# Kernel optimization log

Measured on AMD Instinct MI355X. Metric: run time of the kernel, lower is better.

Reference implementation:

```python
import jax, jax.numpy as jnp
import numpy as np

# JAX reference for BERN-NN-Implicit LayerModule.forward.
# Semantics: for each output node i,
#   combined_over[i]  = sum_j relu(W)[i,j]*inputs_over[j] + (-relu(-W))[i,j]*inputs_under[j] + bias[i]
#   combined_under[i] = sum_j (-relu(-W))[i,j]*inputs_over[j] + relu(W)[i,j]*inputs_under[j] + bias[i]
# With all input Bernstein polynomials at equal degree, SumModule reduces to addition
# and prod_input_weights reduces to a weighted sum over the previous-layer neuron axis.

N_IN = 64      # previous-layer neurons
SIZE = 64      # nodes in this layer
G = 513        # Bernstein coefficient grid per dim (degree 512 + 1), dims = 2


def setup_inputs() -> dict:
    key = jax.random.key(0)
    k1, k2, k3, k4 = jax.random.split(key, 4)
    return {
        "inputs_under": jax.random.normal(k1, (N_IN, G, G), dtype=jnp.float32),
        "inputs_over": jax.random.normal(k2, (N_IN, G, G), dtype=jnp.float32),
        "weights": jax.random.normal(k3, (SIZE, N_IN), dtype=jnp.float32),
        "biases": jax.random.normal(k4, (SIZE,), dtype=jnp.float32),
        "layer_idx": 0,
    }


def reference(inputs_under, inputs_over, weights, biases, layer_idx):
    w_pos = jax.nn.relu(weights)          # [size, n_in]
    w_neg = -jax.nn.relu(-weights)        # [size, n_in]
    b = biases[:, None, None]             # [size, 1, 1]
    # [size, G, G] Bernstein coefficient grids per output node
    combined_over = (jnp.einsum("oi,ixy->oxy", w_pos, inputs_over)
                     + jnp.einsum("oi,ixy->oxy", w_neg, inputs_under)) + b
    combined_under = (jnp.einsum("oi,ixy->oxy", w_neg, inputs_over)
                      + jnp.einsum("oi,ixy->oxy", w_pos, inputs_under)) + b
    return combined_under, combined_over
```

## Files before the change

kernel.cpp:

```cpp
#include <hip/hip_runtime.h>

constexpr int PIX   = 513 * 513;
constexpr int NTILE = 128;

typedef short bf16x8 __attribute__((ext_vector_type(8)));
typedef float f32x4  __attribute__((ext_vector_type(4)));

__device__ unsigned short g_Wbig[128 * 128];

__device__ __forceinline__ unsigned short f2bf(float f) {
    unsigned u = __builtin_bit_cast(unsigned, f);
    u += 0x7fffu + ((u >> 16) & 1u);
    return (unsigned short)(u >> 16);
}
__device__ __forceinline__ unsigned pack2(float a, float b) {
    return (unsigned)f2bf(a) | ((unsigned)f2bf(b) << 16);
}

__global__ __launch_bounds__(256) void prep_kernel(const float* __restrict__ W) {
    const int idx = blockIdx.x * 256 + threadIdx.x;
    const int m = idx >> 7, k = idx & 127;
    const float w = W[(m & 63) * 64 + (k & 63)];
    const bool same = ((m < 64) == (k < 64));
    g_Wbig[idx] = f2bf(same ? fmaxf(w, 0.f) : fminf(w, 0.f));
}

__global__ __launch_bounds__(512, 4) void mfma_bounds_kernel(
    const float* __restrict__ under,
    const float* __restrict__ over,
    const float* __restrict__ W,
    const float* __restrict__ bias,
    float* __restrict__ out_under,
    float* __restrict__ out_over)
{
    __shared__ alignas(16) unsigned short Xt[NTILE * 128];

    const int t = threadIdx.x;
    const int pxbase = blockIdx.x * NTILE;

    if (pxbase + NTILE > PIX) {
        if (t < 128) {
            const int m = t;
            const int o = m & 63;
            const float* prim = (m < 64) ? over  : under;
            const float* sec  = (m < 64) ? under : over;
            for (int p = pxbase; p < PIX; ++p) {
                float acc = bias[o];
                for (int i = 0; i < 64; ++i) {
                    const float w = W[o * 64 + i];
                    acc += fmaxf(w, 0.f) * prim[(size_t)i * PIX + p]
                         + fminf(w, 0.f) * sec [(size_t)i * PIX + p];
                }
                if (m < 64) out_over [(size_t)m        * PIX + p] = acc;
                else        out_under[(size_t)(m - 64) * PIX + p] = acc;
            }
        }
        return;
    }

    {
        const int px = t & 127;
        const int kq = t >> 7;
        const float* src = (kq < 2) ? over : under;
        const int rbase = (kq & 1) * 32;
        const size_t p = (size_t)pxbase + px;
        const int xw = (px & 7) << 4;
        #pragma unroll
        for (int j = 0; j < 4; ++j) {
            const int r0 = rbase + j * 8;
            float v0 = src[(size_t)(r0 + 0) * PIX + p];
            float v1 = src[(size_t)(r0 + 1) * PIX + p];
            float v2 = src[(size_t)(r0 + 2) * PIX + p];
            float v3 = src[(size_t)(r0 + 3) * PIX + p];
            float v4 = src[(size_t)(r0 + 4) * PIX + p];
            float v5 = src[(size_t)(r0 + 5) * PIX + p];
            float v6 = src[(size_t)(r0 + 6) * PIX + p];
            float v7 = src[(size_t)(r0 + 7) * PIX + p];
            int4 pk;
            pk.x = (int)pack2(v0, v1);
            pk.y = (int)pack2(v2, v3);
            pk.z = (int)pack2(v4, v5);
            pk.w = (int)pack2(v6, v7);
            const int off = px * 256 + ((kq * 64 + j * 16) ^ xw);
            *(int4*)((char*)Xt + off) = pk;
        }
    }

    const int wv   = t >> 6;
    const int lane = t & 63;
    const int lrow = lane & 15;
    const int lg   = lane >> 4;
    const int m0   = wv * 16;

    bf16x8 A[4];
    #pragma unroll
    for (int ks = 0; ks < 4; ++ks)
        A[ks] = *(const bf16x8*)&g_Wbig[(m0 + lrow) * 128 + ks * 32 + lg * 8];

    float bb[4];
    #pragma unroll
    for (int r = 0; r < 4; ++r)
        bb[r] = bias[(m0 + lg * 4 + r) & 63];

    __syncthreads();

    const int xwr = (lrow & 7) << 4;

    f32x4 acc[8];
    #pragma unroll
    for (int nt = 0; nt < 8; ++nt) {
        f32x4 v = {bb[0], bb[1], bb[2], bb[3]};
        acc[nt] = v;
    }

    #pragma unroll
    for (int nt = 0; nt < 8; ++nt) {
        const int prow = nt * 16 + lrow;
        bf16x8 Bf[4];
        #pragma unroll
        for (int ks = 0; ks < 4; ++ks) {
            const int ch = ks * 4 + lg;
            Bf[ks] = *(const bf16x8*)((const char*)Xt + prow * 256 + ((ch * 16) ^ xwr));
        }
        #pragma unroll
        for (int ks = 0; ks < 4; ++ks)
            acc[nt] = __builtin_amdgcn_mfma_f32_16x16x32_bf16(A[ks], Bf[ks], acc[nt], 0, 0, 0);
    }

    #pragma unroll
    for (int r = 0; r < 4; ++r) {
        const int m = m0 + lg * 4 + r;
        float* base = (m < 64) ? (out_over  + (size_t)m        * PIX)
                               : (out_under + (size_t)(m - 64) * PIX);
        #pragma unroll
        for (int nt = 0; nt < 8; ++nt)
            __builtin_nontemporal_store(acc[nt][r], base + pxbase + nt * 16 + lrow);
    }
}

extern "C" void kernel_launch(void* const* d_in, const int* in_sizes, int n_in,
                              void* d_out, int out_size, void* d_ws, size_t ws_size,
                              hipStream_t stream) {
    const float* under = (const float*)d_in[0];
    const float* over  = (const float*)d_in[1];
    const float* W     = (const float*)d_in[2];
    const float* bias  = (const float*)d_in[3];
    float* out_under = (float*)d_out;
    float* out_over  = out_under + (size_t)64 * PIX;

    prep_kernel<<<64, 256, 0, stream>>>(W);

    const int blocks = (PIX + NTILE - 1) / NTILE;
    mfma_bounds_kernel<<<blocks, 512, 0, stream>>>(under, over, W, bias,
                                                   out_under, out_over);
}
```

Before: 80.86 us.

## Halve block size, give each wave two M tiles, vectorize input loads

The block shrinks from 512 to 256 threads. Each wave now computes 32 output rows (two 16-row M tiles), so every B fragment read from shared memory feeds twice as many MFMAs. The global-to-shared staging switches from scalar per-pixel loads to 16-byte float4 loads of 4 adjacent pixels across 16 rows, repacked into the same swizzled bf16 layout. This aims to cut load instruction count and LDS read traffic. In exchange, register pressure rises (64 staged floats plus 64 accumulators), and the float4 loads can be misaligned because the row stride of 513*513 floats is odd.

```diff
diff --git a/kernel.cpp b/kernel.cpp
--- a/kernel.cpp
+++ b/kernel.cpp
@@ -25,7 +25,7 @@
     g_Wbig[idx] = f2bf(same ? fmaxf(w, 0.f) : fminf(w, 0.f));
 }
 
-__global__ __launch_bounds__(512, 4) void mfma_bounds_kernel(
+__global__ __launch_bounds__(256, 2) void mfma_bounds_kernel(
     const float* __restrict__ under,
     const float* __restrict__ over,
     const float* __restrict__ W,
@@ -59,30 +59,33 @@
     }
 
     {
-        const int px = t & 127;
-        const int kq = t >> 7;
-        const float* src = (kq < 2) ? over : under;
-        const int rbase = (kq & 1) * 32;
-        const size_t p = (size_t)pxbase + px;
-        const int xw = (px & 7) << 4;
+        const int q   = t & 31;
+        const int ro  = t >> 5;
+        const float* src = (ro < 4) ? over : under;
+        const int rr  = (ro & 3) * 16;
+        const int px0 = q * 4;
+        const size_t pb = (size_t)pxbase + px0;
+
+        f32x4 ld[16];
         #pragma unroll
-        for (int j = 0; j < 4; ++j) {
-            const int r0 = rbase + j * 8;
-            float v0 = src[(size_t)(r0 + 0) * PIX + p];
-            float v1 = src[(size_t)(r0 + 1) * PIX + p];
-            float v2 = src[(size_t)(r0 + 2) * PIX + p];
-            float v3 = src[(size_t)(r0 + 3) * PIX + p];
-            float v4 = src[(size_t)(r0 + 4) * PIX + p];
-            float v5 = src[(size_t)(r0 + 5) * PIX + p];
-            float v6 = src[(size_t)(r0 + 6) * PIX + p];
-            float v7 = src[(size_t)(r0 + 7) * PIX + p];
-            int4 pk;
-            pk.x = (int)pack2(v0, v1);
-            pk.y = (int)pack2(v2, v3);
-            pk.z = (int)pack2(v4, v5);
-            pk.w = (int)pack2(v6, v7);
-            const int off = px * 256 + ((kq * 64 + j * 16) ^ xw);
-            *(int4*)((char*)Xt + off) = pk;
+        for (int j = 0; j < 16; ++j)
+            ld[j] = *(const f32x4*)(src + (size_t)(rr + j) * PIX + pb);
+
+        #pragma unroll
+        for (int c = 0; c < 4; ++c) {
+            const int px = px0 + c;
+            const int xw = (px & 7) << 4;
+            #pragma unroll
+            for (int oct = 0; oct < 2; ++oct) {
+                int4 pk;
+                pk.x = (int)pack2(ld[oct * 8 + 0][c], ld[oct * 8 + 1][c]);
+                pk.y = (int)pack2(ld[oct * 8 + 2][c], ld[oct * 8 + 3][c]);
+                pk.z = (int)pack2(ld[oct * 8 + 4][c], ld[oct * 8 + 5][c]);
+                pk.w = (int)pack2(ld[oct * 8 + 6][c], ld[oct * 8 + 7][c]);
+                const int kbyte = ro * 32 + oct * 16;
+                const int off = px * 256 + (kbyte ^ xw);
+                *(int4*)((char*)Xt + off) = pk;
+            }
         }
     }
 
@@ -90,28 +93,35 @@
     const int lane = t & 63;
     const int lrow = lane & 15;
     const int lg   = lane >> 4;
-    const int m0   = wv * 16;
+    const int m0   = wv * 32;
 
-    bf16x8 A[4];
+    bf16x8 A[2][4];
     #pragma unroll
-    for (int ks = 0; ks < 4; ++ks)
-        A[ks] = *(const bf16x8*)&g_Wbig[(m0 + lrow) * 128 + ks * 32 + lg * 8];
+    for (int mt = 0; mt < 2; ++mt)
+        #pragma unroll
+        for (int ks = 0; ks < 4; ++ks)
+            A[mt][ks] = *(const bf16x8*)&g_Wbig[(m0 + mt * 16 + lrow) * 128 +
+                                                ks * 32 + lg * 8];
 
-    float bb[4];
+    float bb[2][4];
     #pragma unroll
-    for (int r = 0; r < 4; ++r)
-        bb[r] = bias[(m0 + lg * 4 + r) & 63];
+    for (int mt = 0; mt < 2; ++mt)
+        #pragma unroll
+        for (int r = 0; r < 4; ++r)
+            bb[mt][r] = bias[(m0 + mt * 16 + lg * 4 + r) & 63];
 
     __syncthreads();
 
     const int xwr = (lrow & 7) << 4;
 
-    f32x4 acc[8];
+    f32x4 acc[2][8];
     #pragma unroll
-    for (int nt = 0; nt < 8; ++nt) {
-        f32x4 v = {bb[0], bb[1], bb[2], bb[3]};
-        acc[nt] = v;
-    }
+    for (int mt = 0; mt < 2; ++mt)
+        #pragma unroll
+        for (int nt = 0; nt < 8; ++nt) {
+            f32x4 v = {bb[mt][0], bb[mt][1], bb[mt][2], bb[mt][3]};
+            acc[mt][nt] = v;
+        }
 
     #pragma unroll
     for (int nt = 0; nt < 8; ++nt) {
@@ -123,19 +133,25 @@
             Bf[ks] = *(const bf16x8*)((const char*)Xt + prow * 256 + ((ch * 16) ^ xwr));
         }
         #pragma unroll
-        for (int ks = 0; ks < 4; ++ks)
-            acc[nt] = __builtin_amdgcn_mfma_f32_16x16x32_bf16(A[ks], Bf[ks], acc[nt], 0, 0, 0);
+        for (int mt = 0; mt < 2; ++mt)
+            #pragma unroll
+            for (int ks = 0; ks < 4; ++ks)
+                acc[mt][nt] = __builtin_amdgcn_mfma_f32_16x16x32_bf16(
+                    A[mt][ks], Bf[ks], acc[mt][nt], 0, 0, 0);
     }
 
     #pragma unroll
-    for (int r = 0; r < 4; ++r) {
-        const int m = m0 + lg * 4 + r;
-        float* base = (m < 64) ? (out_over  + (size_t)m        * PIX)
-                               : (out_under + (size_t)(m - 64) * PIX);
+    for (int mt = 0; mt < 2; ++mt)
         #pragma unroll
-        for (int nt = 0; nt < 8; ++nt)
-            __builtin_nontemporal_store(acc[nt][r], base + pxbase + nt * 16 + lrow);
-    }
+        for (int r = 0; r < 4; ++r) {
+            const int m = m0 + mt * 16 + lg * 4 + r;
+            float* base = (m < 64) ? (out_over  + (size_t)m        * PIX)
+                                   : (out_under + (size_t)(m - 64) * PIX);
+            #pragma unroll
+            for (int nt = 0; nt < 8; ++nt)
+                __builtin_nontemporal_store(acc[mt][nt][r],
+                    base + pxbase + nt * 16 + lrow);
+        }
 }
 
 extern "C" void kernel_launch(void* const* d_in, const int* in_sizes, int n_in,
@@ -151,6 +167,6 @@
     prep_kernel<<<64, 256, 0, stream>>>(W);
 
     const int blocks = (PIX + NTILE - 1) / NTILE;
-    mfma_bounds_kernel<<<blocks, 512, 0, stream>>>(under, over, W, bias,
+    mfma_bounds_kernel<<<blocks, 256, 0, stream>>>(under, over, W, bias,
                                                    out_under, out_over);
 }
```

Result: no change. 79.57 us (-1.6%).
